# Kernel tuning notes

Hardware: AMD Instinct MI355X
Metric: run time of the kernel (lower is better)

## Reference

```python
import jax, jax.numpy as jnp
import numpy as np

N_SPK = 2048
M_UTT = 16
D_EMB = 512
EPS = 1e-8  # torch cosine_similarity eps


def setup_inputs() -> dict:
    key = jax.random.key(0)
    k1, = jax.random.split(key, 1)
    speaker_vectors = jax.random.normal(k1, (N_SPK * M_UTT, D_EMB), dtype=jnp.float32)
    return {
        "speaker_vectors": speaker_vectors,
        "w": jnp.float32(10.0),
        "b": jnp.float32(-5.0),
        "speakers": N_SPK,
    }


def _normalize(x):
    # torch.cosine_similarity clamps each norm at eps
    n = jnp.maximum(jnp.linalg.norm(x, axis=-1, keepdims=True), EPS)
    return x / n


def reference(speaker_vectors, w, b, speakers):
    N = speakers
    NM, D = speaker_vectors.shape
    M = NM // N
    v3 = speaker_vectors.reshape(N, M, D)
    ssum = v3.sum(axis=1)                         # [N, D] per-speaker sums
    C = ssum / M                                  # full centroids [N, D]
    C_min = (ssum[:, None, :] - v3) / (M - 1)     # leave-one-out centroids [N, M, D]

    vn = _normalize(speaker_vectors)              # [NM, D]
    # diagonal similarities: cos(C_min[j], v[j]) per utterance j
    S_diag = jnp.sum(_normalize(C_min.reshape(NM, D)) * vn, axis=-1)  # [NM]
    # full similarity matrix via one normalized matmul: [N, NM]
    S_full = _normalize(C) @ vn.T
    # replace each speaker's own block row entries with leave-one-out sims
    col_spk = jnp.arange(NM) // M                 # speaker id of each column
    same = col_spk[None, :] == jnp.arange(N)[:, None]  # [N, NM]
    S = jnp.where(same, S_diag[None, :], S_full)

    # L_j = -(w*S_diag_j + b) + log sum_n exp(w*S[n,j] + b)
    L = -(w * S_diag + b) + jax.nn.logsumexp(w * S + b, axis=0)
    return L.sum()
```

## Files before the change

### kernel.cpp

```cpp
#include <hip/hip_runtime.h>
#include <stdint.h>

#define N_SPK 2048
#define M_UTT 16
#define D_EMB 512
#define NM (N_SPK * M_UTT)
#define FP8_SCALE 16.0f

typedef __attribute__((ext_vector_type(4))) float f32x4;
typedef __attribute__((ext_vector_type(4))) int   i32x4;
typedef __attribute__((ext_vector_type(8))) int   i32x8;

__device__ __forceinline__ void async_copy16(const void* g, void* l) {
    __builtin_amdgcn_global_load_lds(
        (const __attribute__((address_space(1))) unsigned int*)g,
        (__attribute__((address_space(3))) unsigned int*)l,
        16, 0, 0);
}

__device__ __forceinline__ i32x8 ld_frag(const unsigned char* base, int s0) {
    i32x4 lo = *(const i32x4*)(base + s0 * 16);
    i32x4 hi = *(const i32x4*)(base + (s0 ^ 1) * 16);
    return __builtin_shufflevector(lo, hi, 0, 1, 2, 3, 4, 5, 6, 7);
}

__global__ __launch_bounds__(256) void prep_kernel(
    const float* __restrict__ V, const float* __restrict__ wp,
    const float* __restrict__ bp, unsigned char* __restrict__ Cn8,
    unsigned char* __restrict__ vn8, float* __restrict__ dterm,
    float* __restrict__ colsum, float* __restrict__ out)
{
    const int spk = blockIdx.x, t = threadIdx.x;
    const int wave = t >> 6, lane = t & 63;
    const float2* vb = (const float2*)(V + (size_t)spk * (M_UTT * D_EMB));

    __shared__ __align__(16) float red[32][264];
    __shared__ float red2[32];
    __shared__ float invs[M_UTT];
    __shared__ float wred[4];

    if (spk < 128) colsum[spk * 256 + t] = 0.f;
    if (spk == 0 && t == 0) out[0] = 0.f;

    float2 p[M_UTT];
#pragma unroll
    for (int m = 0; m < M_UTT; ++m) p[m] = vb[m * 256 + t];

    float2 ss = make_float2(0.f, 0.f);
#pragma unroll
    for (int m = 0; m < M_UTT; ++m) { ss.x += p[m].x; ss.y += p[m].y; }

    float cnp = ss.x * ss.x + ss.y * ss.y;
#pragma unroll
    for (int off = 32; off > 0; off >>= 1) cnp += __shfl_xor(cnp, off);
    if (lane == 0) wred[wave] = cnp;

#pragma unroll
    for (int m = 0; m < M_UTT; ++m) {
        red[m][t]         = ss.x * p[m].x + ss.y * p[m].y;
        red[m + M_UTT][t] = p[m].x * p[m].x + p[m].y * p[m].y;
    }
    __syncthreads();
    const float cn2 = wred[0] + wred[1] + wred[2] + wred[3];

    {
        const int r = t >> 3, s = t & 7;
        const float4* rp = (const float4*)red;
        float4 a = make_float4(0.f, 0.f, 0.f, 0.f);
#pragma unroll
        for (int k = 0; k < 8; ++k) {
            float4 q = rp[r * 66 + s + 8 * k];
            a.x += q.x; a.y += q.y; a.z += q.z; a.w += q.w;
        }
        float v1 = (a.x + a.y) + (a.z + a.w);
        v1 += __shfl_xor(v1, 1);
        v1 += __shfl_xor(v1, 2);
        v1 += __shfl_xor(v1, 4);
        if (s == 0) red2[r] = v1;
    }
    __syncthreads();

    if (t < M_UTT) {
        const float sv = red2[t], vv = red2[t + M_UTT];
        const float cc = cn2 - 2.f * sv + vv;
        const float cv = sv - vv;
        const float dc = fmaxf(sqrtf(fmaxf(cc, 0.f)) * (1.f / (M_UTT - 1)), 1e-8f) * (M_UTT - 1);
        const float dv = fmaxf(sqrtf(vv), 1e-8f);
        dterm[spk * M_UTT + t] = (*wp) * (cv / (dc * dv)) + (*bp);
        invs[t] = FP8_SCALE / dv;
    }
    __syncthreads();

    const float cs = FP8_SCALE / (M_UTT * fmaxf(sqrtf(cn2) * (1.f / M_UTT), 1e-8f));
    {
        int pk = __builtin_amdgcn_cvt_pk_fp8_f32(ss.x * cs, ss.y * cs, 0, false);
        ((unsigned short*)(Cn8 + (size_t)spk * D_EMB))[t] = (unsigned short)pk;
    }
#pragma unroll
    for (int m = 0; m < M_UTT; ++m) {
        const float iv = invs[m];
        int pk = __builtin_amdgcn_cvt_pk_fp8_f32(p[m].x * iv, p[m].y * iv, 0, false);
        ((unsigned short*)(vn8 + ((size_t)(spk * M_UTT + m)) * D_EMB))[t] = (unsigned short)pk;
    }
}

__global__ __launch_bounds__(256) void gemm_kernel(
    const unsigned char* __restrict__ Cn8, const unsigned char* __restrict__ vn8,
    const float* __restrict__ wp, const float* __restrict__ bp,
    float* __restrict__ colsum)
{
    __shared__ __align__(16) unsigned char As[2 * 128 * 128];
    __shared__ __align__(16) unsigned char Bs[2 * 128 * 128];
    __shared__ float csum[128];

    const int tid = threadIdx.x;
    const int w = tid >> 6, l = tid & 63;

    const int p_lin = blockIdx.x + 16 * blockIdx.y;
    const int L_log = (p_lin & 7) * 512 + (p_lin >> 3);
    const int by = L_log & 15;
    const int bx = L_log >> 4;

    const float wgt = (*wp) * (1.f / (FP8_SCALE * FP8_SCALE));
    const float bsc = *bp;

    if (tid < 128) csum[tid] = 0.f;

    const int r_l = l >> 3, sl8 = l & 7;
    const int g = sl8 ^ r_l;
    const unsigned char* Ab = Cn8 + (size_t)(by * 128 + w * 32 + r_l) * D_EMB + g * 16;
    const unsigned char* Bb = vn8 + (size_t)(bx * 128 + w * 32 + r_l) * D_EMB + g * 16;
    unsigned char* AsW0 = As + (w * 32) * 128;
    unsigned char* BsW0 = Bs + (w * 32) * 128;

    const int wm = w & 1, wn = w >> 1;
    const int l16 = l & 15, q = l >> 4;
    const int s0 = (2 * q) ^ (l & 7);
    const unsigned char* Ard0 = As + (wm * 64 + l16) * 128;
    const unsigned char* Brd0 = Bs + (wn * 64 + l16) * 128;

    f32x4 acc[4][4];
    const f32x4 z = {0.f, 0.f, 0.f, 0.f};
#pragma unroll
    for (int i = 0; i < 4; ++i)
#pragma unroll
        for (int j = 0; j < 4; ++j) acc[i][j] = z;

#define STAGE(kt, b) do {                                                    \
        unsigned char* aw_ = AsW0 + (b) * 16384;                             \
        unsigned char* bw_ = BsW0 + (b) * 16384;                             \
        _Pragma("unroll")                                                    \
        for (int i_ = 0; i_ < 4; ++i_) {                                     \
            async_copy16(Ab + i_ * 4096 + (kt) * 128, aw_ + i_ * 1024);      \
            async_copy16(Bb + i_ * 4096 + (kt) * 128, bw_ + i_ * 1024);      \
        } } while (0)

#define COMPUTE(b) do {                                                      \
        const unsigned char* Ard_ = Ard0 + (b) * 16384;                      \
        const unsigned char* Brd_ = Brd0 + (b) * 16384;                      \
        i32x8 bfr_[4];                                                       \
        _Pragma("unroll")                                                    \
        for (int j_ = 0; j_ < 4; ++j_) bfr_[j_] = ld_frag(Brd_ + j_ * 2048, s0); \
        _Pragma("unroll")                                                    \
        for (int i_ = 0; i_ < 4; ++i_) {                                     \
            i32x8 af_ = ld_frag(Ard_ + i_ * 2048, s0);                       \
            _Pragma("unroll")                                                \
            for (int j_ = 0; j_ < 4; ++j_)                                   \
                acc[i_][j_] = __builtin_amdgcn_mfma_scale_f32_16x16x128_f8f6f4( \
                    af_, bfr_[j_], acc[i_][j_], 0, 0, 0, 0x7F7F7F7F, 0, 0x7F7F7F7F); \
        } } while (0)

    STAGE(0, 0);
    STAGE(1, 1);

    asm volatile("s_waitcnt vmcnt(8)" ::: "memory");
    __builtin_amdgcn_s_barrier();
    __builtin_amdgcn_sched_barrier(0);
    COMPUTE(0);
    __builtin_amdgcn_sched_barrier(0);
    __builtin_amdgcn_s_barrier();
    __builtin_amdgcn_sched_barrier(0);
    STAGE(2, 0);

    asm volatile("s_waitcnt vmcnt(8)" ::: "memory");
    __builtin_amdgcn_s_barrier();
    __builtin_amdgcn_sched_barrier(0);
    COMPUTE(1);
    __builtin_amdgcn_sched_barrier(0);
    __builtin_amdgcn_s_barrier();
    __builtin_amdgcn_sched_barrier(0);
    STAGE(3, 1);

    asm volatile("s_waitcnt vmcnt(8)" ::: "memory");
    __builtin_amdgcn_s_barrier();
    __builtin_amdgcn_sched_barrier(0);
    COMPUTE(0);

    asm volatile("s_waitcnt vmcnt(0)" ::: "memory");
    __builtin_amdgcn_s_barrier();
    __builtin_amdgcn_sched_barrier(0);
    COMPUTE(1);

#undef STAGE
#undef COMPUTE

    const int rowg0 = by * 128 + wm * 64 + q * 4;
    const int colg0 = bx * 128 + wn * 64 + l16;
#pragma unroll
    for (int j = 0; j < 4; ++j) {
        const int colg = colg0 + j * 16;
        const int cspk = colg >> 4;
        float p = 0.f;
#pragma unroll
        for (int i = 0; i < 4; ++i) {
            const int rowg = rowg0 + i * 16;
#pragma unroll
            for (int r = 0; r < 4; ++r) {
                float e = __expf(wgt * acc[i][j][r] + bsc);
                p += (rowg + r == cspk) ? 0.f : e;
            }
        }
        p += __shfl_xor(p, 16);
        p += __shfl_xor(p, 32);
        if (q == 0) atomicAdd(&csum[wn * 64 + j * 16 + l16], p);
    }
    __syncthreads();
    if (tid < 128) atomicAdd(&colsum[bx * 128 + tid], csum[tid]);
}

__global__ __launch_bounds__(256) void finish_kernel(
    const float* __restrict__ dterm, const float* __restrict__ colsum,
    float* __restrict__ out)
{
    const int idx = blockIdx.x * 256 + threadIdx.x;
    const int stride = gridDim.x * 256;
    float local = 0.f;
    for (int j = idx; j < NM; j += stride) {
        float t = dterm[j];
        local += logf(colsum[j] + __expf(t)) - t;
    }
#pragma unroll
    for (int off = 32; off > 0; off >>= 1) local += __shfl_xor(local, off);
    __shared__ float wr[4];
    const int wave = threadIdx.x >> 6, lane = threadIdx.x & 63;
    if (lane == 0) wr[wave] = local;
    __syncthreads();
    if (threadIdx.x == 0) atomicAdd(out, wr[0] + wr[1] + wr[2] + wr[3]);
}

extern "C" void kernel_launch(void* const* d_in, const int* in_sizes, int n_in,
                              void* d_out, int out_size, void* d_ws, size_t ws_size,
                              hipStream_t stream) {
    const float* V  = (const float*)d_in[0];
    const float* wp = (const float*)d_in[1];
    const float* bp = (const float*)d_in[2];

    char* ws = (char*)d_ws;
    unsigned char* Cn8 = (unsigned char*)ws;
    unsigned char* vn8 = (unsigned char*)(ws + ((size_t)1 << 20));
    float* dterm  = (float*)(ws + ((size_t)17 << 20));
    float* colsum = dterm + NM;
    float* out    = (float*)d_out;

    prep_kernel<<<N_SPK, 256, 0, stream>>>(V, wp, bp, Cn8, vn8, dterm, colsum, out);
    gemm_kernel<<<dim3(N_SPK / 128, NM / 128), 256, 0, stream>>>(Cn8, vn8, wp, bp, colsum);
    finish_kernel<<<64, 256, 0, stream>>>(dterm, colsum, out);
}
```

Before: 148.6 us.

## Enlarge GEMM tile to 256x256 with 8 waves and MFMA priority hints

The GEMM block grows from a 128x128 tile with 4 waves to a 256x256 tile with 512 threads. Each wave now computes a 128x64 sub-tile, which raises operand reuse per LDS fragment load and cuts the block count. MFMA phases are wrapped in s_setprio, and the explicit sched_barriers are removed so the compiler can interleave work more freely. The prep kernel's per-utterance reduction is repacked into float2 pairs. In exchange, the block uses about 128KB of LDS and 128 accumulator registers per lane. With launch_bounds(512,2), that risks register spills and a single resident block per CU.

```diff
diff --git a/kernel.cpp b/kernel.cpp
--- a/kernel.cpp
+++ b/kernel.cpp
@@ -34,7 +34,7 @@
     const int wave = t >> 6, lane = t & 63;
     const float2* vb = (const float2*)(V + (size_t)spk * (M_UTT * D_EMB));
 
-    __shared__ __align__(16) float red[32][264];
+    __shared__ __align__(16) float2 red[M_UTT][264];
     __shared__ float red2[32];
     __shared__ float invs[M_UTT];
     __shared__ float wred[4];
@@ -57,31 +57,32 @@
 
 #pragma unroll
     for (int m = 0; m < M_UTT; ++m) {
-        red[m][t]         = ss.x * p[m].x + ss.y * p[m].y;
-        red[m + M_UTT][t] = p[m].x * p[m].x + p[m].y * p[m].y;
+        red[m][t] = make_float2(ss.x * p[m].x + ss.y * p[m].y,
+                                p[m].x * p[m].x + p[m].y * p[m].y);
     }
     __syncthreads();
     const float cn2 = wred[0] + wred[1] + wred[2] + wred[3];
 
     {
-        const int r = t >> 3, s = t & 7;
+        const int r = t >> 4, s = t & 15;
         const float4* rp = (const float4*)red;
-        float4 a = make_float4(0.f, 0.f, 0.f, 0.f);
+        float sv = 0.f, vvs = 0.f;
 #pragma unroll
         for (int k = 0; k < 8; ++k) {
-            float4 q = rp[r * 66 + s + 8 * k];
-            a.x += q.x; a.y += q.y; a.z += q.z; a.w += q.w;
+            float4 q = rp[r * 132 + s + 16 * k];
+            sv  += q.x + q.z;
+            vvs += q.y + q.w;
         }
-        float v1 = (a.x + a.y) + (a.z + a.w);
-        v1 += __shfl_xor(v1, 1);
-        v1 += __shfl_xor(v1, 2);
-        v1 += __shfl_xor(v1, 4);
-        if (s == 0) red2[r] = v1;
+        sv  += __shfl_xor(sv, 1);  vvs += __shfl_xor(vvs, 1);
+        sv  += __shfl_xor(sv, 2);  vvs += __shfl_xor(vvs, 2);
+        sv  += __shfl_xor(sv, 4);  vvs += __shfl_xor(vvs, 4);
+        sv  += __shfl_xor(sv, 8);  vvs += __shfl_xor(vvs, 8);
+        if (s == 0) { red2[r] = sv; red2[r + 16] = vvs; }
     }
     __syncthreads();
 
     if (t < M_UTT) {
-        const float sv = red2[t], vv = red2[t + M_UTT];
+        const float sv = red2[t], vv = red2[t + 16];
         const float cc = cn2 - 2.f * sv + vv;
         const float cv = sv - vv;
         const float dc = fmaxf(sqrtf(fmaxf(cc, 0.f)) * (1.f / (M_UTT - 1)), 1e-8f) * (M_UTT - 1);
@@ -104,115 +105,117 @@
     }
 }
 
-__global__ __launch_bounds__(256) void gemm_kernel(
+__global__ __launch_bounds__(512, 2) void gemm_kernel(
     const unsigned char* __restrict__ Cn8, const unsigned char* __restrict__ vn8,
     const float* __restrict__ wp, const float* __restrict__ bp,
     float* __restrict__ colsum)
 {
-    __shared__ __align__(16) unsigned char As[2 * 128 * 128];
-    __shared__ __align__(16) unsigned char Bs[2 * 128 * 128];
-    __shared__ float csum[128];
+    __shared__ __align__(16) unsigned char As[2 * 256 * 128];
+    __shared__ __align__(16) unsigned char Bs[2 * 256 * 128];
+    __shared__ float csum[256];
 
     const int tid = threadIdx.x;
     const int w = tid >> 6, l = tid & 63;
 
-    const int p_lin = blockIdx.x + 16 * blockIdx.y;
-    const int L_log = (p_lin & 7) * 512 + (p_lin >> 3);
-    const int by = L_log & 15;
-    const int bx = L_log >> 4;
+    const int p_lin = blockIdx.x + 8 * blockIdx.y;
+    const int L_log = (p_lin & 7) * 128 + (p_lin >> 3);
+    const int by = L_log & 7;
+    const int bx = L_log >> 3;
 
     const float wgt = (*wp) * (1.f / (FP8_SCALE * FP8_SCALE));
     const float bsc = *bp;
 
-    if (tid < 128) csum[tid] = 0.f;
+    if (tid < 256) csum[tid] = 0.f;
 
     const int r_l = l >> 3, sl8 = l & 7;
     const int g = sl8 ^ r_l;
-    const unsigned char* Ab = Cn8 + (size_t)(by * 128 + w * 32 + r_l) * D_EMB + g * 16;
-    const unsigned char* Bb = vn8 + (size_t)(bx * 128 + w * 32 + r_l) * D_EMB + g * 16;
+    const unsigned char* Ab = Cn8 + (size_t)(by * 256 + w * 32 + r_l) * D_EMB + g * 16;
+    const unsigned char* Bb = vn8 + (size_t)(bx * 256 + w * 32 + r_l) * D_EMB + g * 16;
     unsigned char* AsW0 = As + (w * 32) * 128;
     unsigned char* BsW0 = Bs + (w * 32) * 128;
 
     const int wm = w & 1, wn = w >> 1;
     const int l16 = l & 15, q = l >> 4;
     const int s0 = (2 * q) ^ (l & 7);
-    const unsigned char* Ard0 = As + (wm * 64 + l16) * 128;
+    const unsigned char* Ard0 = As + (wm * 128 + l16) * 128;
     const unsigned char* Brd0 = Bs + (wn * 64 + l16) * 128;
 
-    f32x4 acc[4][4];
+    f32x4 acc[8][4];
     const f32x4 z = {0.f, 0.f, 0.f, 0.f};
 #pragma unroll
-    for (int i = 0; i < 4; ++i)
+    for (int i = 0; i < 8; ++i)
 #pragma unroll
         for (int j = 0; j < 4; ++j) acc[i][j] = z;
 
 #define STAGE(kt, b) do {                                                    \
-        unsigned char* aw_ = AsW0 + (b) * 16384;                             \
-        unsigned char* bw_ = BsW0 + (b) * 16384;                             \
+        unsigned char* aw_ = AsW0 + (b) * 32768;                             \
+        unsigned char* bw_ = BsW0 + (b) * 32768;                             \
         _Pragma("unroll")                                                    \
         for (int i_ = 0; i_ < 4; ++i_) {                                     \
             async_copy16(Ab + i_ * 4096 + (kt) * 128, aw_ + i_ * 1024);      \
             async_copy16(Bb + i_ * 4096 + (kt) * 128, bw_ + i_ * 1024);      \
         } } while (0)
 
+#define PHASE(i0) do {                                                       \
+        i32x8 af0_ = ld_frag(Ard_ + (i0) * 2048, s0);                        \
+        i32x8 af1_ = ld_frag(Ard_ + ((i0) + 1) * 2048, s0);                  \
+        __builtin_amdgcn_s_setprio(1);                                       \
+        _Pragma("unroll")                                                    \
+        for (int j_ = 0; j_ < 4; ++j_)                                       \
+            acc[i0][j_] = __builtin_amdgcn_mfma_scale_f32_16x16x128_f8f6f4(  \
+                af0_, bfr_[j_], acc[i0][j_], 0, 0, 0, 0x7F7F7F7F, 0, 0x7F7F7F7F); \
+        _Pragma("unroll")                                                    \
+        for (int j_ = 0; j_ < 4; ++j_)                                       \
+            acc[(i0)+1][j_] = __builtin_amdgcn_mfma_scale_f32_16x16x128_f8f6f4( \
+                af1_, bfr_[j_], acc[(i0)+1][j_], 0, 0, 0, 0x7F7F7F7F, 0, 0x7F7F7F7F); \
+        __builtin_amdgcn_s_setprio(0);                                       \
+    } while (0)
+
 #define COMPUTE(b) do {                                                      \
-        const unsigned char* Ard_ = Ard0 + (b) * 16384;                      \
-        const unsigned char* Brd_ = Brd0 + (b) * 16384;                      \
+        const unsigned char* Ard_ = Ard0 + (b) * 32768;                      \
+        const unsigned char* Brd_ = Brd0 + (b) * 32768;                      \
         i32x8 bfr_[4];                                                       \
         _Pragma("unroll")                                                    \
         for (int j_ = 0; j_ < 4; ++j_) bfr_[j_] = ld_frag(Brd_ + j_ * 2048, s0); \
-        _Pragma("unroll")                                                    \
-        for (int i_ = 0; i_ < 4; ++i_) {                                     \
-            i32x8 af_ = ld_frag(Ard_ + i_ * 2048, s0);                       \
-            _Pragma("unroll")                                                \
-            for (int j_ = 0; j_ < 4; ++j_)                                   \
-                acc[i_][j_] = __builtin_amdgcn_mfma_scale_f32_16x16x128_f8f6f4( \
-                    af_, bfr_[j_], acc[i_][j_], 0, 0, 0, 0x7F7F7F7F, 0, 0x7F7F7F7F); \
-        } } while (0)
+        PHASE(0); PHASE(2); PHASE(4); PHASE(6);                              \
+    } while (0)
 
     STAGE(0, 0);
     STAGE(1, 1);
 
     asm volatile("s_waitcnt vmcnt(8)" ::: "memory");
     __builtin_amdgcn_s_barrier();
-    __builtin_amdgcn_sched_barrier(0);
     COMPUTE(0);
-    __builtin_amdgcn_sched_barrier(0);
-    __builtin_amdgcn_s_barrier();
-    __builtin_amdgcn_sched_barrier(0);
+    __builtin_amdgcn_s_barrier();
     STAGE(2, 0);
 
     asm volatile("s_waitcnt vmcnt(8)" ::: "memory");
     __builtin_amdgcn_s_barrier();
-    __builtin_amdgcn_sched_barrier(0);
     COMPUTE(1);
-    __builtin_amdgcn_sched_barrier(0);
-    __builtin_amdgcn_s_barrier();
-    __builtin_amdgcn_sched_barrier(0);
+    __builtin_amdgcn_s_barrier();
     STAGE(3, 1);
 
     asm volatile("s_waitcnt vmcnt(8)" ::: "memory");
     __builtin_amdgcn_s_barrier();
-    __builtin_amdgcn_sched_barrier(0);
     COMPUTE(0);
 
     asm volatile("s_waitcnt vmcnt(0)" ::: "memory");
     __builtin_amdgcn_s_barrier();
-    __builtin_amdgcn_sched_barrier(0);
     COMPUTE(1);
 
 #undef STAGE
+#undef PHASE
 #undef COMPUTE
 
-    const int rowg0 = by * 128 + wm * 64 + q * 4;
-    const int colg0 = bx * 128 + wn * 64 + l16;
+    const int rowg0 = by * 256 + wm * 128 + q * 4;
+    const int colg0 = bx * 256 + wn * 64 + l16;
 #pragma unroll
     for (int j = 0; j < 4; ++j) {
         const int colg = colg0 + j * 16;
         const int cspk = colg >> 4;
         float p = 0.f;
 #pragma unroll
-        for (int i = 0; i < 4; ++i) {
+        for (int i = 0; i < 8; ++i) {
             const int rowg = rowg0 + i * 16;
 #pragma unroll
             for (int r = 0; r < 4; ++r) {
@@ -225,7 +228,7 @@
         if (q == 0) atomicAdd(&csum[wn * 64 + j * 16 + l16], p);
     }
     __syncthreads();
-    if (tid < 128) atomicAdd(&colsum[bx * 128 + tid], csum[tid]);
+    if (tid < 256) atomicAdd(&colsum[bx * 256 + tid], csum[tid]);
 }
 
 __global__ __launch_bounds__(256) void finish_kernel(
@@ -263,6 +266,6 @@
     float* out    = (float*)d_out;
 
     prep_kernel<<<N_SPK, 256, 0, stream>>>(V, wp, bp, Cn8, vn8, dterm, colsum, out);
-    gemm_kernel<<<dim3(N_SPK / 128, NM / 128), 256, 0, stream>>>(Cn8, vn8, wp, bp, colsum);
+    gemm_kernel<<<dim3(8, 128), 512, 0, stream>>>(Cn8, vn8, wp, bp, colsum);
     finish_kernel<<<64, 256, 0, stream>>>(dterm, colsum, out);
 }
```

Result: slower. 181.2 us (+21.9%).
